# Optimization experiments

Hardware: AMD Instinct MI355X
Metric: run time of the kernel (lower is better)

## Reference

```python
import jax, jax.numpy as jnp
import numpy as np

NUM_GROUPS = 8
IN_FEATURES = 4096
OUT_FEATURES = 4096
TOTAL_TOKENS = 16384  # divisible by NUM_GROUPS


def setup_inputs() -> dict:
    key = jax.random.key(0)
    kx, kw = jax.random.split(key)
    x = jax.random.normal(kx, (TOTAL_TOKENS, IN_FEATURES), dtype=jnp.float32)
    weight = jax.random.normal(kw, (NUM_GROUPS, IN_FEATURES, OUT_FEATURES), dtype=jnp.float32)
    return {"x": x, "weight": weight}


def reference(x, weight):
    # split -> per-group matmul -> cat  ==  batched (grouped) GEMM
    g, i, o = weight.shape
    xg = x.reshape(g, x.shape[0] // g, i)          # [G, B/G, I]
    out = jnp.einsum("gbi,gio->gbo", xg, weight)   # [G, B/G, O]
    return out.reshape(x.shape[0], o)              # cat along dim 0
```

## Files before the change

kernel.cpp:

```cpp
#include <hip/hip_runtime.h>


#define K_DIM 4096
#define N_DIM 4096
#define M_TOT 16384
#define GROUPS 8

typedef __bf16 bf16x8 __attribute__((ext_vector_type(8)));
typedef float f32x4 __attribute__((ext_vector_type(4)));

__device__ __forceinline__ unsigned short f2bf(float f) {
  unsigned int u = __builtin_bit_cast(unsigned int, f);
  return (unsigned short)((u + 0x7FFFu + ((u >> 16) & 1u)) >> 16);
}

#define GLOAD_LDS16(gp, lp)                                          \
  __builtin_amdgcn_global_load_lds(                                  \
      (__attribute__((address_space(1))) void*)(void*)(gp),          \
      (__attribute__((address_space(3))) void*)(void*)(lp), 16, 0, 0)

__global__ __launch_bounds__(256) void cvt_x_kernel(const float* __restrict__ x,
                                                    unsigned short* __restrict__ xb) {
  size_t i = (size_t)blockIdx.x * 256 + threadIdx.x;
  const float4* in = (const float4*)x;
  float4 a = in[2 * i];
  float4 b = in[2 * i + 1];
  uint4 o;
  o.x = (unsigned)f2bf(a.x) | ((unsigned)f2bf(a.y) << 16);
  o.y = (unsigned)f2bf(a.z) | ((unsigned)f2bf(a.w) << 16);
  o.z = (unsigned)f2bf(b.x) | ((unsigned)f2bf(b.y) << 16);
  o.w = (unsigned)f2bf(b.z) | ((unsigned)f2bf(b.w) << 16);
  ((uint4*)xb)[i] = o;
}

__global__ __launch_bounds__(256) void cvt_wT_kernel(const float* __restrict__ w,
                                                     unsigned short* __restrict__ wt) {
  __shared__ unsigned short tile[64][65];
  const size_t base = (size_t)blockIdx.z * K_DIM * N_DIM;
  const int n0 = blockIdx.x * 64;
  const int k0 = blockIdx.y * 64;
  const int tx = threadIdx.x & 15;
  const int ty = threadIdx.x >> 4;
#pragma unroll
  for (int i = 0; i < 4; ++i) {
    int k = ty + i * 16;
    float4 v = *(const float4*)&w[base + (size_t)(k0 + k) * N_DIM + n0 + tx * 4];
    tile[k][tx * 4 + 0] = f2bf(v.x);
    tile[k][tx * 4 + 1] = f2bf(v.y);
    tile[k][tx * 4 + 2] = f2bf(v.z);
    tile[k][tx * 4 + 3] = f2bf(v.w);
  }
  __syncthreads();
  const int kx = threadIdx.x & 7;
  const int ny = threadIdx.x >> 3;
#pragma unroll
  for (int i = 0; i < 2; ++i) {
    int n = ny + i * 32;
    uint4 o;
    o.x = (unsigned)tile[kx * 8 + 0][n] | ((unsigned)tile[kx * 8 + 1][n] << 16);
    o.y = (unsigned)tile[kx * 8 + 2][n] | ((unsigned)tile[kx * 8 + 3][n] << 16);
    o.z = (unsigned)tile[kx * 8 + 4][n] | ((unsigned)tile[kx * 8 + 5][n] << 16);
    o.w = (unsigned)tile[kx * 8 + 6][n] | ((unsigned)tile[kx * 8 + 7][n] << 16);
    *(uint4*)&wt[base + (size_t)(n0 + n) * K_DIM + k0 + kx * 8] = o;
  }
}

__device__ __forceinline__ void mfma_tile(const unsigned short* sA, const unsigned short* sB,
                                          f32x4 acc[4][4], int wm, int wn, int fr, int fk) {
  bf16x8 af[4], bb[4];
#pragma unroll
  for (int t = 0; t < 4; ++t) {
    af[t] = *(const bf16x8*)&sA[(wm + t * 16 + fr) * 32 + fk];
    bb[t] = *(const bf16x8*)&sB[(wn + t * 16 + fr) * 32 + fk];
  }
#pragma unroll
  for (int i = 0; i < 4; ++i)
#pragma unroll
    for (int j = 0; j < 4; ++j)
      acc[i][j] = __builtin_amdgcn_mfma_f32_16x16x32_bf16(af[i], bb[j], acc[i][j], 0, 0, 0);
}

__device__ __forceinline__ void epilogue(float* __restrict__ C, f32x4 acc[4][4],
                                         int tm0, int tn0, int wm, int wn, int lane) {
  const int rr = (lane >> 4) * 4;
  const int cc = lane & 15;
#pragma unroll
  for (int i = 0; i < 4; ++i)
#pragma unroll
    for (int j = 0; j < 4; ++j) {
      size_t row = (size_t)(tm0 + wm + i * 16 + rr);
      size_t col = (size_t)(tn0 + wn + j * 16 + cc);
#pragma unroll
      for (int r = 0; r < 4; ++r) C[(row + r) * N_DIM + col] = acc[i][j][r];
    }
}

__global__ __launch_bounds__(256) void gemm_bt_kernel(const unsigned short* __restrict__ A,
                                                      const unsigned short* __restrict__ BT,
                                                      float* __restrict__ C) {
  __shared__ unsigned short sA[128 * 32];
  __shared__ unsigned short sB[128 * 32];
  const int tn0 = blockIdx.x * 128;
  const int tm0 = blockIdx.y * 128;
  const int g = blockIdx.y >> 4;
  const unsigned short* Bg = BT + (size_t)g * K_DIM * N_DIM;

  const int lane = threadIdx.x & 63;
  const int wave = threadIdx.x >> 6;
  const int wm = (wave >> 1) * 64;
  const int wn = (wave & 1) * 64;

  const int srow = wave * 16 + (lane >> 2);
  const int scol = (lane & 3) * 8;
  const unsigned short* gA0 = A + (size_t)(tm0 + srow) * K_DIM + scol;
  const unsigned short* gA1 = A + (size_t)(tm0 + 64 + srow) * K_DIM + scol;
  const unsigned short* gB0 = Bg + (size_t)(tn0 + srow) * K_DIM + scol;
  const unsigned short* gB1 = Bg + (size_t)(tn0 + 64 + srow) * K_DIM + scol;
  unsigned short* lA0 = &sA[(wave * 16) * 32];
  unsigned short* lA1 = &sA[(64 + wave * 16) * 32];
  unsigned short* lB0 = &sB[(wave * 16) * 32];
  unsigned short* lB1 = &sB[(64 + wave * 16) * 32];

  f32x4 acc[4][4];
#pragma unroll
  for (int i = 0; i < 4; ++i)
#pragma unroll
    for (int j = 0; j < 4; ++j) acc[i][j] = (f32x4){0.f, 0.f, 0.f, 0.f};

  const int fr = lane & 15;
  const int fk = (lane >> 4) * 8;

  for (int k0 = 0; k0 < K_DIM; k0 += 32) {
    GLOAD_LDS16(gA0 + k0, lA0);
    GLOAD_LDS16(gA1 + k0, lA1);
    GLOAD_LDS16(gB0 + k0, lB0);
    GLOAD_LDS16(gB1 + k0, lB1);
    __syncthreads();
    mfma_tile(sA, sB, acc, wm, wn, fr, fk);
    __syncthreads();
  }
  epilogue(C, acc, tm0, tn0, wm, wn, lane);
}

__global__ __launch_bounds__(256) void gemm_fused_kernel(const float* __restrict__ X,
                                                         const float* __restrict__ W,
                                                         float* __restrict__ C) {
  __shared__ unsigned short sA[128 * 32];
  __shared__ unsigned short sB[128 * 32];
  const int tn0 = blockIdx.x * 128;
  const int tm0 = blockIdx.y * 128;
  const int g = blockIdx.y >> 4;
  const float* Wg = W + (size_t)g * K_DIM * N_DIM;
  const int tid = threadIdx.x;
  const int lane = tid & 63, wave = tid >> 6;
  const int wm = (wave >> 1) * 64, wn = (wave & 1) * 64;
  const int fr = lane & 15, fk = (lane >> 4) * 8;

  const int ac = (tid & 7) * 4;
  const int ar = tid >> 3;
  const int bn = (tid & 31) * 4;
  const int bk = tid >> 5;

  f32x4 acc[4][4];
#pragma unroll
  for (int i = 0; i < 4; ++i)
#pragma unroll
    for (int j = 0; j < 4; ++j) acc[i][j] = (f32x4){0.f, 0.f, 0.f, 0.f};

  for (int k0 = 0; k0 < K_DIM; k0 += 32) {
    float4 av[4], bv[4];
#pragma unroll
    for (int p = 0; p < 4; ++p)
      av[p] = *(const float4*)&X[(size_t)(tm0 + ar + p * 32) * K_DIM + k0 + ac];
#pragma unroll
    for (int p = 0; p < 4; ++p)
      bv[p] = *(const float4*)&Wg[(size_t)(k0 + bk + p * 8) * N_DIM + tn0 + bn];
#pragma unroll
    for (int p = 0; p < 4; ++p) {
      ushort4 s;
      s.x = f2bf(av[p].x); s.y = f2bf(av[p].y); s.z = f2bf(av[p].z); s.w = f2bf(av[p].w);
      *(ushort4*)&sA[(ar + p * 32) * 32 + ac] = s;
    }
#pragma unroll
    for (int p = 0; p < 4; ++p) {
      sB[(bn + 0) * 32 + bk + p * 8] = f2bf(bv[p].x);
      sB[(bn + 1) * 32 + bk + p * 8] = f2bf(bv[p].y);
      sB[(bn + 2) * 32 + bk + p * 8] = f2bf(bv[p].z);
      sB[(bn + 3) * 32 + bk + p * 8] = f2bf(bv[p].w);
    }
    __syncthreads();
    mfma_tile(sA, sB, acc, wm, wn, fr, fk);
    __syncthreads();
  }
  epilogue(C, acc, tm0, tn0, wm, wn, lane);
}

extern "C" void kernel_launch(void* const* d_in, const int* in_sizes, int n_in,
                              void* d_out, int out_size, void* d_ws, size_t ws_size,
                              hipStream_t stream) {
  const float* x = (const float*)d_in[0];
  const float* w = (const float*)d_in[1];
  float* out = (float*)d_out;
  const size_t xe = (size_t)M_TOT * K_DIM;
  const size_t we = (size_t)GROUPS * K_DIM * N_DIM;
  const size_t need = (xe + we) * sizeof(unsigned short);

  if (ws_size >= need) {
    unsigned short* xb = (unsigned short*)d_ws;
    unsigned short* wt = xb + xe;
    cvt_x_kernel<<<dim3((unsigned)(xe / (256 * 8))), 256, 0, stream>>>(x, xb);
    cvt_wT_kernel<<<dim3(N_DIM / 64, K_DIM / 64, GROUPS), 256, 0, stream>>>(w, wt);
    gemm_bt_kernel<<<dim3(N_DIM / 128, M_TOT / 128), 256, 0, stream>>>(xb, wt, out);
  } else {
    gemm_fused_kernel<<<dim3(N_DIM / 128, M_TOT / 128), 256, 0, stream>>>(x, w, out);
  }
}
```

Baseline: 1.796 ms.

## Replace 128x128 GEMM with 256x256 multi-stage pipelined swizzled-LDS kernel

```diff
diff --git a/kernel.cpp b/kernel.cpp
--- a/kernel.cpp
+++ b/kernel.cpp
@@ -65,6 +65,106 @@
   }
 }
 
+
+#define STAGE2(gp, matofs, B_, KS_, T_) do {                                   \
+    const unsigned short* _g = (gp) + (size_t)(T_) * 64 + (KS_) * 32;          \
+    unsigned short* _l = &lds[(((B_) * 4 + (matofs) + (KS_)) * 8192) + ldw];   \
+    GLOAD_LDS16(_g, _l);                                                       \
+    GLOAD_LDS16(_g + (size_t)128 * K_DIM, _l + 4096);                          \
+  } while (0)
+
+#define PHASE8(B_, KS_, QH_, LOADB_, STAGE_STMT, VM_STMT) do {                 \
+    const int _ab = ((B_) * 4 + (KS_)) * 8192;                                 \
+    const int _bb = ((B_) * 4 + 2 + (KS_)) * 8192;                             \
+    _Pragma("unroll") for (int _i = 0; _i < 4; ++_i)                           \
+      af[_i] = *(const bf16x8*)&lds[_ab + (wm + (QH_) * 64 + _i * 16 + fr) * 32 + pc8]; \
+    if (LOADB_) {                                                              \
+      _Pragma("unroll") for (int _i = 0; _i < 4; ++_i)                         \
+        bfr[_i] = *(const bf16x8*)&lds[_bb + (wn + _i * 16 + fr) * 32 + pc8];  \
+    }                                                                          \
+    STAGE_STMT;                                                                \
+    __builtin_amdgcn_s_barrier();                                              \
+    asm volatile("s_waitcnt lgkmcnt(0)" ::: "memory");                         \
+    __builtin_amdgcn_sched_barrier(0);                                         \
+    __builtin_amdgcn_s_setprio(1);                                             \
+    _Pragma("unroll") for (int _i = 0; _i < 4; ++_i)                           \
+      _Pragma("unroll") for (int _j = 0; _j < 4; ++_j)                         \
+        acc[(QH_) * 4 + _i][_j] = __builtin_amdgcn_mfma_f32_16x16x32_bf16(     \
+            af[_i], bfr[_j], acc[(QH_) * 4 + _i][_j], 0, 0, 0);                \
+    __builtin_amdgcn_s_setprio(0);                                             \
+    VM_STMT;                                                                   \
+    __builtin_amdgcn_s_barrier();                                              \
+  } while (0)
+
+__global__ __launch_bounds__(512, 2) void gemm_bt256_kernel(
+    const unsigned short* __restrict__ A, const unsigned short* __restrict__ BT,
+    float* __restrict__ C) {
+  __shared__ unsigned short lds[65536];
+
+  const int id = blockIdx.x;
+  const int swz = (id & 7) * 128 + (id >> 3);
+  const int tm0 = (swz >> 4) * 256;
+  const int tn0 = (swz & 15) * 256;
+  const int g = swz >> 7;
+  const unsigned short* Bg = BT + (size_t)g * ((size_t)K_DIM * N_DIM);
+
+  const int tid = threadIdx.x;
+  const int lane = tid & 63;
+  const int wave = tid >> 6;
+  const int wm = (wave >> 2) * 128;
+  const int wn = (wave & 3) * 64;
+  const int fr = lane & 15;
+  const int pc8 = ((lane >> 4) ^ ((fr >> 1) & 3)) * 8;
+
+  const int srow = tid >> 2;
+  const int schunk = ((tid & 3) ^ ((tid >> 3) & 3)) * 8;
+  const unsigned short* pA = A + (size_t)(tm0 + srow) * K_DIM + schunk;
+  const unsigned short* pB = Bg + (size_t)(tn0 + srow) * K_DIM + schunk;
+  const int ldw = wave * 512;
+
+  f32x4 acc[8][4];
+#pragma unroll
+  for (int i = 0; i < 8; ++i)
+#pragma unroll
+    for (int j = 0; j < 4; ++j) acc[i][j] = (f32x4){0.f, 0.f, 0.f, 0.f};
+  bf16x8 af[4], bfr[4];
+
+  STAGE2(pA, 0, 0, 0, 0);
+  STAGE2(pB, 2, 0, 0, 0);
+  STAGE2(pA, 0, 0, 1, 0);
+  STAGE2(pB, 2, 0, 1, 0);
+  STAGE2(pA, 0, 1, 0, 1);
+  STAGE2(pB, 2, 1, 0, 1);
+  asm volatile("s_waitcnt vmcnt(4)" ::: "memory");
+  __builtin_amdgcn_s_barrier();
+
+  for (int t = 0; t < 64; t += 2) {
+    PHASE8(0, 0, 0, 1, { STAGE2(pA, 0, 1, 1, t + 1); }, {});
+    PHASE8(0, 0, 1, 0, { STAGE2(pB, 2, 1, 1, t + 1); }, {});
+    PHASE8(0, 1, 0, 1, { if (t < 62) STAGE2(pA, 0, 0, 0, t + 2); }, {});
+    PHASE8(0, 1, 1, 0, { if (t < 62) STAGE2(pB, 2, 0, 0, t + 2); },
+           { if (t < 62) asm volatile("s_waitcnt vmcnt(4)" ::: "memory");
+             else        asm volatile("s_waitcnt vmcnt(0)" ::: "memory"); });
+    PHASE8(1, 0, 0, 1, { if (t < 62) STAGE2(pA, 0, 0, 1, t + 2); }, {});
+    PHASE8(1, 0, 1, 0, { if (t < 62) STAGE2(pB, 2, 0, 1, t + 2); }, {});
+    PHASE8(1, 1, 0, 1, { if (t < 62) STAGE2(pA, 0, 1, 0, t + 3); }, {});
+    PHASE8(1, 1, 1, 0, { if (t < 62) STAGE2(pB, 2, 1, 0, t + 3); },
+           { if (t < 62) asm volatile("s_waitcnt vmcnt(4)" ::: "memory"); });
+  }
+
+  const int rr = (lane >> 4) * 4;
+  const int cc = lane & 15;
+#pragma unroll
+  for (int mi = 0; mi < 8; ++mi)
+#pragma unroll
+    for (int ni = 0; ni < 4; ++ni) {
+      size_t row = (size_t)(tm0 + wm + mi * 16 + rr);
+      size_t col = (size_t)(tn0 + wn + ni * 16 + cc);
+#pragma unroll
+      for (int r = 0; r < 4; ++r) C[(row + r) * N_DIM + col] = acc[mi][ni][r];
+    }
+}
+
 __device__ __forceinline__ void mfma_tile(const unsigned short* sA, const unsigned short* sB,
                                           f32x4 acc[4][4], int wm, int wn, int fr, int fk) {
   bf16x8 af[4], bb[4];
@@ -93,53 +193,6 @@
 #pragma unroll
       for (int r = 0; r < 4; ++r) C[(row + r) * N_DIM + col] = acc[i][j][r];
     }
-}
-
-__global__ __launch_bounds__(256) void gemm_bt_kernel(const unsigned short* __restrict__ A,
-                                                      const unsigned short* __restrict__ BT,
-                                                      float* __restrict__ C) {
-  __shared__ unsigned short sA[128 * 32];
-  __shared__ unsigned short sB[128 * 32];
-  const int tn0 = blockIdx.x * 128;
-  const int tm0 = blockIdx.y * 128;
-  const int g = blockIdx.y >> 4;
-  const unsigned short* Bg = BT + (size_t)g * K_DIM * N_DIM;
-
-  const int lane = threadIdx.x & 63;
-  const int wave = threadIdx.x >> 6;
-  const int wm = (wave >> 1) * 64;
-  const int wn = (wave & 1) * 64;
-
-  const int srow = wave * 16 + (lane >> 2);
-  const int scol = (lane & 3) * 8;
-  const unsigned short* gA0 = A + (size_t)(tm0 + srow) * K_DIM + scol;
-  const unsigned short* gA1 = A + (size_t)(tm0 + 64 + srow) * K_DIM + scol;
-  const unsigned short* gB0 = Bg + (size_t)(tn0 + srow) * K_DIM + scol;
-  const unsigned short* gB1 = Bg + (size_t)(tn0 + 64 + srow) * K_DIM + scol;
-  unsigned short* lA0 = &sA[(wave * 16) * 32];
-  unsigned short* lA1 = &sA[(64 + wave * 16) * 32];
-  unsigned short* lB0 = &sB[(wave * 16) * 32];
-  unsigned short* lB1 = &sB[(64 + wave * 16) * 32];
-
-  f32x4 acc[4][4];
-#pragma unroll
-  for (int i = 0; i < 4; ++i)
-#pragma unroll
-    for (int j = 0; j < 4; ++j) acc[i][j] = (f32x4){0.f, 0.f, 0.f, 0.f};
-
-  const int fr = lane & 15;
-  const int fk = (lane >> 4) * 8;
-
-  for (int k0 = 0; k0 < K_DIM; k0 += 32) {
-    GLOAD_LDS16(gA0 + k0, lA0);
-    GLOAD_LDS16(gA1 + k0, lA1);
-    GLOAD_LDS16(gB0 + k0, lB0);
-    GLOAD_LDS16(gB1 + k0, lB1);
-    __syncthreads();
-    mfma_tile(sA, sB, acc, wm, wn, fr, fk);
-    __syncthreads();
-  }
-  epilogue(C, acc, tm0, tn0, wm, wn, lane);
 }
 
 __global__ __launch_bounds__(256) void gemm_fused_kernel(const float* __restrict__ X,
@@ -210,7 +263,7 @@
     unsigned short* wt = xb + xe;
     cvt_x_kernel<<<dim3((unsigned)(xe / (256 * 8))), 256, 0, stream>>>(x, xb);
     cvt_wT_kernel<<<dim3(N_DIM / 64, K_DIM / 64, GROUPS), 256, 0, stream>>>(w, wt);
-    gemm_bt_kernel<<<dim3(N_DIM / 128, M_TOT / 128), 256, 0, stream>>>(xb, wt, out);
+    gemm_bt256_kernel<<<dim3(16 * (M_TOT / 256)), dim3(512), 0, stream>>>(xb, wt, out);
   } else {
     gemm_fused_kernel<<<dim3(N_DIM / 128, M_TOT / 128), 256, 0, stream>>>(x, w, out);
   }
```

Result: faster. 1.439 ms (-19.9%).
